# Optimization experiments

Measured on AMD Instinct MI355X. Metric: run time of the kernel, lower is better.

The kernel has to match this reference:

```python
import jax, jax.numpy as jnp
import numpy as np

EMBED_DIM = 512
NUM_TYPES = 26
PER_TYPE = 128
NUM_CODES = NUM_TYPES * PER_TYPE
COMMIT = 0.25
TEMP = 0.07
N_TOKENS = 32768
SAMPLED_PER_TYPE = int(0.1 * PER_TYPE)  # 12


def _normalize(v, axis=-1):
    # matches F.normalize(p=2) with eps clamp
    return v / jnp.clip(jnp.linalg.norm(v, axis=axis, keepdims=True), 1e-12)


def setup_inputs() -> dict:
    key = jax.random.key(0)
    k1, k2, k3, k4 = jax.random.split(key, 4)
    x = jax.random.normal(k1, (N_TOKENS, EMBED_DIM), jnp.float32)
    Q = jax.random.randint(k2, (N_TOKENS,), 0, NUM_TYPES)
    initrange = 1.0 / EMBED_DIM
    emb = jax.random.uniform(k3, (NUM_CODES, EMBED_DIM), jnp.float32, -initrange, initrange)
    emb = _normalize(emb)  # mirrors _initialize_embeddings
    # deterministic stand-in for torch.randperm(num_per_type)[:sampled_num]
    perm = jax.random.permutation(k4, PER_TYPE)[:SAMPLED_PER_TYPE]
    sampled_indices = (jnp.arange(NUM_TYPES)[:, None] * PER_TYPE + perm[None, :]).reshape(-1)
    return {"x": x, "embeddings": emb, "Q": Q, "sampled_indices": sampled_indices}


def _code_indices(xn, embeddings, Q):
    # full [N, num_codes] squared distances, then select the 128-code slab of
    # each token's PTM type and argmin within it (equivalent to the per-type loop)
    d = ((xn ** 2).sum(-1, keepdims=True)
         + (embeddings ** 2).sum(-1)[None, :]
         - 2.0 * (xn @ embeddings.T))                      # [N, NUM_CODES]
    d = d.reshape(xn.shape[0], NUM_TYPES, PER_TYPE)
    d_sel = jnp.take_along_axis(d, Q[:, None, None], axis=1)[:, 0, :]  # [N, PER_TYPE]
    return jnp.argmin(d_sel, axis=1) + Q * PER_TYPE


def _uniform_loss(embeddings, sampled_indices):
    ne = _normalize(embeddings)
    se = ne[sampled_indices]                               # [S, D]
    sim = se @ se.T                                        # [S, S]
    labels = sampled_indices // PER_TYPE
    pos = (labels[None, :] == labels[:, None]).astype(jnp.float32)
    S = sampled_indices.shape[0]
    eye = jnp.eye(S, dtype=bool)
    sim = jnp.where(eye, -jnp.inf, sim)
    sim_exp = jnp.exp(sim / TEMP)                          # exp(-inf) = 0 kills diagonal
    sum_exp = sim_exp.sum(axis=1)
    pos_sum = (sim_exp * pos).sum(axis=1)
    return -jnp.log(pos_sum / sum_exp).mean()


def reference(x, embeddings, Q, sampled_indices):
    xn = _normalize(x)
    idx = _code_indices(xn, embeddings, Q)
    quantized = _normalize(embeddings[idx])
    q_latent = jnp.mean((quantized - jax.lax.stop_gradient(xn)) ** 2)
    e_latent = jnp.mean((xn - jax.lax.stop_gradient(quantized)) ** 2)
    loss = q_latent + COMMIT * e_latent
    uloss = _uniform_loss(embeddings, sampled_indices)
    out = xn + jax.lax.stop_gradient(quantized - xn)       # straight-through
    return out, loss, uloss, idx
```

## Files before the change

### kernel.cpp

```cpp
#include <hip/hip_runtime.h>
#include <math.h>

#define NTOK   32768
#define DIM    512
#define NTYPES 26
#define PT     128
#define NCODES 3328
#define NSAMP  312
#define INV_TEMP (1.0f / 0.07f)
#define MAXTILES 24

typedef __attribute__((ext_vector_type(8))) short short8;
typedef __attribute__((ext_vector_type(4))) float floatx4;

__device__ __forceinline__ void f2bf2(float f, unsigned short& h, unsigned short& l) {
    unsigned u = __float_as_uint(f);
    unsigned hb = (u + 0x7fffu + ((u >> 16) & 1u)) >> 16;
    h = (unsigned short)hb;
    float hf = __uint_as_float(hb << 16);
    float r = f - hf;
    unsigned u2 = __float_as_uint(r);
    l = (unsigned short)((u2 + 0x7fffu + ((u2 >> 16) & 1u)) >> 16);
}

__device__ __forceinline__ void cvt8(float4 a, float4 b, short8& h, short8& l) {
    union { short8 v; unsigned short u[8]; } H, L;
    f2bf2(a.x, H.u[0], L.u[0]); f2bf2(a.y, H.u[1], L.u[1]);
    f2bf2(a.z, H.u[2], L.u[2]); f2bf2(a.w, H.u[3], L.u[3]);
    f2bf2(b.x, H.u[4], L.u[4]); f2bf2(b.y, H.u[5], L.u[5]);
    f2bf2(b.z, H.u[6], L.u[6]); f2bf2(b.w, H.u[7], L.u[7]);
    h = H.v; l = L.v;
}

__device__ __forceinline__ void stage2(const unsigned short* g, unsigned short* l) {
    __builtin_amdgcn_global_load_lds((const __attribute__((address_space(1))) void*)g,
                                     (__attribute__((address_space(3))) void*)l, 16, 0, 0);
    __builtin_amdgcn_global_load_lds((const __attribute__((address_space(1))) void*)(g + 512),
                                     (__attribute__((address_space(3))) void*)(l + 512), 16, 0, 0);
}

__global__ __launch_bounds__(256) void k_pre(const float* __restrict__ emb,
                                             const int* __restrict__ Q,
                                             unsigned short* __restrict__ Bhg,
                                             unsigned short* __restrict__ Blg,
                                             float* __restrict__ sume,
                                             float* __restrict__ rinv,
                                             int* __restrict__ bhist,
                                             int* __restrict__ rankb,
                                             float* __restrict__ accg,
                                             int* __restrict__ donec) {
    int tid = threadIdx.x;
    int bid = blockIdx.x;
    if (bid < NCODES / 4) {
        if (bid == 0) {
            if (tid == 32) accg[0] = 0.0f;
            if (tid == 33) accg[1] = 0.0f;
            if (tid == 34) *donec = 0;
        }
        int wv = tid >> 6, lane = tid & 63;
        int c = bid * 4 + wv;
        const float4* row = (const float4*)(emb + (size_t)c * DIM);
        float4 v0 = row[lane * 2], v1 = row[lane * 2 + 1];
        float s = v0.x*v0.x + v0.y*v0.y + v0.z*v0.z + v0.w*v0.w
                + v1.x*v1.x + v1.y*v1.y + v1.z*v1.z + v1.w*v1.w;
        for (int m = 32; m; m >>= 1) s += __shfl_xor(s, m);
        if (lane == 0) {
            sume[c] = s;
            rinv[c] = 1.0f / fmaxf(sqrtf(s), 1e-12f);
        }
        union { short8 v; unsigned short u[8]; } hh, ll;
        f2bf2(v0.x, hh.u[0], ll.u[0]); f2bf2(v0.y, hh.u[1], ll.u[1]);
        f2bf2(v0.z, hh.u[2], ll.u[2]); f2bf2(v0.w, hh.u[3], ll.u[3]);
        f2bf2(v1.x, hh.u[4], ll.u[4]); f2bf2(v1.y, hh.u[5], ll.u[5]);
        f2bf2(v1.z, hh.u[6], ll.u[6]); f2bf2(v1.w, hh.u[7], ll.u[7]);
        int qq  = c >> 7;
        int n   = c & 127;
        int ni  = n >> 4, lcc = n & 15;
        int ks2 = lane >> 2, q4d = lane & 3;
        size_t dst = (size_t)qq * (PT * DIM)
                   + (size_t)(((ks2 * 8 + ni) * 64 + q4d * 16 + lcc) * 8);
        *(short8*)(Bhg + dst) = hh.v;
        *(short8*)(Blg + dst) = ll.v;
    } else {
        __shared__ int lbin[NTYPES];
        int hb = bid - NCODES / 4;
        if (tid < NTYPES) lbin[tid] = 0;
        __syncthreads();
        int t = hb * 256 + tid;
        int q = Q[t];
        int lr = atomicAdd(&lbin[q], 1);
        __syncthreads();
        if (tid < NTYPES) bhist[hb * 32 + tid] = lbin[tid];
        rankb[t] = lr;
    }
}

__global__ __launch_bounds__(256) void k_scat(const int* __restrict__ Q,
                                              const int* __restrict__ bhist,
                                              const int* __restrict__ rankb,
                                              int* __restrict__ order,
                                              int* __restrict__ offsg) {
    __shared__ int offs_s[NTYPES];
    __shared__ int base_s[NTYPES];
    int b = blockIdx.x;
    int tid = threadIdx.x;
    if (tid < NTYPES) {
        int tot = 0, pre = 0;
        for (int bb = 0; bb < NTOK / 256; bb++) {
            int v = bhist[bb * 32 + tid];
            tot += v;
            if (bb < b) pre += v;
        }
        offs_s[tid] = tot;
        base_s[tid] = pre;
    }
    __syncthreads();
    if (tid == 0) {
        int a = 0;
        for (int t2 = 0; t2 < NTYPES; t2++) {
            int tt = offs_s[t2];
            offs_s[t2] = a;
            if (b == 0) offsg[t2] = a;
            a += tt;
        }
        if (b == 0) offsg[NTYPES] = a;
    }
    __syncthreads();
    int t = b * 256 + tid;
    int q = Q[t];
    order[offs_s[q] + base_s[q] + rankb[t]] = t;
}

#define KSTEP(S, NSTR, AC, AF, DOSTAGE)                                          \
  {                                                                              \
    __builtin_amdgcn_sched_barrier(0);                                           \
    asm volatile("s_waitcnt vmcnt(" NSTR ")" ::: "memory");                      \
    __builtin_amdgcn_s_barrier();                                                \
    __builtin_amdgcn_sched_barrier(0);                                           \
    if (DOSTAGE) {                                                               \
      stage2(bhg + ((S) + 2) * 4096 + stoff, &Bls[((S) + 2) % 3][0][ldoff]);     \
      stage2(blg + ((S) + 2) * 4096 + stoff, &Bls[((S) + 2) % 3][1][ldoff]);     \
      AF[0] = *(const float4*)(ap0 + ((S) + 2) * 32);                            \
      AF[1] = *(const float4*)(ap0 + ((S) + 2) * 32 + 4);                        \
      AF[2] = *(const float4*)(ap1 + ((S) + 2) * 32);                            \
      AF[3] = *(const float4*)(ap1 + ((S) + 2) * 32 + 4);                        \
    }                                                                            \
    __builtin_amdgcn_sched_barrier(0);                                           \
    {                                                                            \
      float4 r0a = AC[0], r0b = AC[1], r1a = AC[2], r1b = AC[3];                 \
      ps0 = fmaf(r0a.x, r0a.x, fmaf(r0a.y, r0a.y, fmaf(r0a.z, r0a.z, fmaf(r0a.w, r0a.w, ps0)))); \
      ps0 = fmaf(r0b.x, r0b.x, fmaf(r0b.y, r0b.y, fmaf(r0b.z, r0b.z, fmaf(r0b.w, r0b.w, ps0)))); \
      ps1 = fmaf(r1a.x, r1a.x, fmaf(r1a.y, r1a.y, fmaf(r1a.z, r1a.z, fmaf(r1a.w, r1a.w, ps1)))); \
      ps1 = fmaf(r1b.x, r1b.x, fmaf(r1b.y, r1b.y, fmaf(r1b.z, r1b.z, fmaf(r1b.w, r1b.w, ps1)))); \
      short8 ah0, al0, ah1, al1;                                                 \
      cvt8(r0a, r0b, ah0, al0);                                                  \
      cvt8(r1a, r1b, ah1, al1);                                                  \
      short8 bhf[4], blf[4];                                                     \
      _Pragma("unroll")                                                          \
      for (int ni = 0; ni < 4; ni++) {                                           \
        bhf[ni] = *(const short8*)&Bls[(S) % 3][0][(wn4 + ni) * 512 + lane8];    \
        blf[ni] = *(const short8*)&Bls[(S) % 3][1][(wn4 + ni) * 512 + lane8];    \
      }                                                                          \
      _Pragma("unroll")                                                          \
      for (int ni = 0; ni < 4; ni++) {                                           \
        acc[0][ni] = __builtin_amdgcn_mfma_f32_16x16x32_bf16(ah0, bhf[ni], acc[0][ni], 0, 0, 0); \
        acc[0][ni] = __builtin_amdgcn_mfma_f32_16x16x32_bf16(ah0, blf[ni], acc[0][ni], 0, 0, 0); \
        acc[0][ni] = __builtin_amdgcn_mfma_f32_16x16x32_bf16(al0, bhf[ni], acc[0][ni], 0, 0, 0); \
        acc[1][ni] = __builtin_amdgcn_mfma_f32_16x16x32_bf16(ah1, bhf[ni], acc[1][ni], 0, 0, 0); \
        acc[1][ni] = __builtin_amdgcn_mfma_f32_16x16x32_bf16(ah1, blf[ni], acc[1][ni], 0, 0, 0); \
        acc[1][ni] = __builtin_amdgcn_mfma_f32_16x16x32_bf16(al1, bhf[ni], acc[1][ni], 0, 0, 0); \
      }                                                                          \
    }                                                                            \
  }

__global__ __launch_bounds__(256, 3) void k_main(const float* __restrict__ x,
                                                 const float* __restrict__ emb,
                                                 const unsigned short* __restrict__ Bhg,
                                                 const unsigned short* __restrict__ Blg,
                                                 const int* __restrict__ order,
                                                 const int* __restrict__ offsg,
                                                 const float* __restrict__ sume,
                                                 const float* __restrict__ rinv,
                                                 float* __restrict__ outbuf,
                                                 float* __restrict__ idxout,
                                                 float* __restrict__ accg) {
    int q = blockIdx.x;
    int tile = blockIdx.y;
    int base = offsg[q];
    int cnt = offsg[q + 1] - base;
    int tstart = tile * 64;
    if (tstart >= cnt) return;
    int nt = min(64, cnt - tstart);

    __shared__ unsigned short Bls[3][2][4096];
    __shared__ int   toks_s[64];
    __shared__ float sume_s[128];
    __shared__ float rinv_s[128];
    __shared__ float redv[64][2];
    __shared__ int   redi[64][2];
    __shared__ int   bestc[64];

    int tid = threadIdx.x;
    int lane = tid & 63;
    int wv = tid >> 6;
    int wm = wv & 1, wn = wv >> 1;
    int lc = lane & 15, q4 = lane >> 4;
    int wn4 = wn * 4, lane8 = lane * 8;
    int stoff = wv * 1024 + lane8;
    int ldoff = wv * 1024;

    if (tid < 64) toks_s[tid] = order[base + tstart + min(tid, nt - 1)];
    if (tid < 128) {
        sume_s[tid] = sume[q * PT + tid];
        rinv_s[tid] = rinv[q * PT + tid];
    }

    int row0 = wm * 32 + lc;
    int tok0 = order[base + tstart + min(row0, nt - 1)];
    int tok1 = order[base + tstart + min(row0 + 16, nt - 1)];
    const float* ap0 = x + (size_t)tok0 * DIM + q4 * 8;
    const float* ap1 = x + (size_t)tok1 * DIM + q4 * 8;

    const unsigned short* bhg = Bhg + (size_t)q * (PT * DIM);
    const unsigned short* blg = Blg + (size_t)q * (PT * DIM);

    floatx4 acc[2][4];
#pragma unroll
    for (int mi = 0; mi < 2; mi++)
#pragma unroll
        for (int ni = 0; ni < 4; ni++)
            acc[mi][ni] = (floatx4){0.f, 0.f, 0.f, 0.f};
    float ps0 = 0.f, ps1 = 0.f;
    float4 Aa[4], Ab[4], Ac[4];

    stage2(bhg + stoff, &Bls[0][0][ldoff]);
    stage2(blg + stoff, &Bls[0][1][ldoff]);
    __builtin_amdgcn_sched_barrier(0);
    Aa[0] = *(const float4*)(ap0);      Aa[1] = *(const float4*)(ap0 + 4);
    Aa[2] = *(const float4*)(ap1);      Aa[3] = *(const float4*)(ap1 + 4);
    __builtin_amdgcn_sched_barrier(0);
    stage2(bhg + 4096 + stoff, &Bls[1][0][ldoff]);
    stage2(blg + 4096 + stoff, &Bls[1][1][ldoff]);
    __builtin_amdgcn_sched_barrier(0);
    Ab[0] = *(const float4*)(ap0 + 32); Ab[1] = *(const float4*)(ap0 + 36);
    Ab[2] = *(const float4*)(ap1 + 32); Ab[3] = *(const float4*)(ap1 + 36);

    KSTEP(0,  "8", Aa, Ac, 1)
    KSTEP(1,  "8", Ab, Aa, 1)
    KSTEP(2,  "8", Ac, Ab, 1)
    KSTEP(3,  "8", Aa, Ac, 1)
    KSTEP(4,  "8", Ab, Aa, 1)
    KSTEP(5,  "8", Ac, Ab, 1)
    KSTEP(6,  "8", Aa, Ac, 1)
    KSTEP(7,  "8", Ab, Aa, 1)
    KSTEP(8,  "8", Ac, Ab, 1)
    KSTEP(9,  "8", Aa, Ac, 1)
    KSTEP(10, "8", Ab, Aa, 1)
    KSTEP(11, "8", Ac, Ab, 1)
    KSTEP(12, "8", Aa, Ac, 1)
    KSTEP(13, "8", Ab, Aa, 1)
    KSTEP(14, "8", Ac, Ab, 0)
    KSTEP(15, "0", Aa, Ab, 0)

    ps0 += __shfl_xor(ps0, 16); ps0 += __shfl_xor(ps0, 32);
    ps1 += __shfl_xor(ps1, 16); ps1 += __shfl_xor(ps1, 32);
    float rn0 = 1.0f / fmaxf(sqrtf(ps0), 1e-12f);
    float rn1 = 1.0f / fmaxf(sqrtf(ps1), 1e-12f);

#pragma unroll
    for (int mi = 0; mi < 2; mi++) {
#pragma unroll
        for (int r = 0; r < 4; r++) {
            int rowrel = q4 * 4 + r;
            float rn = __shfl(mi == 0 ? rn0 : rn1, rowrel);
            float rn2v = -2.0f * rn;
            float bv = 1e30f; int bc = 0;
#pragma unroll
            for (int ni = 0; ni < 4; ni++) {
                int n = wn * 64 + ni * 16 + lc;
                float d = fmaf(rn2v, acc[mi][ni][r], sume_s[n]);
                if (d < bv) { bv = d; bc = n; }
            }
#pragma unroll
            for (int mk = 1; mk <= 8; mk <<= 1) {
                float ov = __shfl_xor(bv, mk);
                int oc = __shfl_xor(bc, mk);
                if (ov < bv || (ov == bv && oc < bc)) { bv = ov; bc = oc; }
            }
            int m = wm * 32 + mi * 16 + rowrel;
            if (lc == 0) { redv[m][wn] = bv; redi[m][wn] = bc; }
        }
    }
    __syncthreads();

    if (tid < 64) {
        float v0 = redv[tid][0], v1 = redv[tid][1];
        int c = (v1 < v0) ? redi[tid][1] : redi[tid][0];
        float bvv = fminf(v0, v1);
        bestc[tid] = c;
        float term = 0.0f;
        if (tid < nt) {
            idxout[toks_s[tid]] = (float)(q * PT + c);
            term = 2.0f - (sume_s[c] - bvv) * rinv_s[c];
        }
        for (int mk = 32; mk; mk >>= 1) term += __shfl_xor(term, mk);
        if (tid == 0) atomicAdd(&accg[0], term);
    }
    __syncthreads();

    for (int t = wv; t < nt; t += 4) {
        int c = bestc[t];
        int gt = toks_s[t];
        float rv = rinv_s[c];
        const float4* er = (const float4*)(emb + (size_t)(q * PT + c) * DIM);
        float4* orow = (float4*)(outbuf + (size_t)gt * DIM);
#pragma unroll
        for (int s2 = 0; s2 < 2; s2++) {
            float4 ev = er[lane * 2 + s2];
            orow[lane * 2 + s2] = make_float4(ev.x * rv, ev.y * rv, ev.z * rv, ev.w * rv);
        }
    }
}

__global__ __launch_bounds__(256) void k_post(const float* __restrict__ emb,
                                              const int* __restrict__ samp,
                                              const float* __restrict__ rinv,
                                              float* __restrict__ accg,
                                              int* __restrict__ donec,
                                              float* __restrict__ lossp) {
    __shared__ float rs[4], rp[4];
    int i = blockIdx.x;
    int tid = threadIdx.x;
    int lane = tid & 63, wv = tid >> 6;
    int ci = samp[i];
    float rvi = rinv[ci];
    int labi = ci >> 7;
    const float4* ri = (const float4*)(emb + (size_t)ci * DIM);
    float4 e0 = ri[lane * 2], e1 = ri[lane * 2 + 1];
    float sE = 0.0f, pE = 0.0f;
    for (int j0 = wv; j0 < NSAMP; j0 += 16) {
        float d[4]; int cj[4]; bool val[4];
#pragma unroll
        for (int u = 0; u < 4; u++) {
            int j = j0 + u * 4;
            val[u] = (j < NSAMP) && (j != i);
            int js = val[u] ? j : 0;
            cj[u] = samp[js];
            const float4* rj = (const float4*)(emb + (size_t)cj[u] * DIM);
            float4 f0 = rj[lane * 2], f1 = rj[lane * 2 + 1];
            d[u] = e0.x*f0.x + e0.y*f0.y + e0.z*f0.z + e0.w*f0.w
                 + e1.x*f1.x + e1.y*f1.y + e1.z*f1.z + e1.w*f1.w;
        }
#pragma unroll
        for (int mk = 32; mk; mk >>= 1)
#pragma unroll
            for (int u = 0; u < 4; u++) d[u] += __shfl_xor(d[u], mk);
#pragma unroll
        for (int u = 0; u < 4; u++) {
            float ex = val[u] ? expf(d[u] * rvi * rinv[cj[u]] * INV_TEMP) : 0.0f;
            sE += ex;
            if (val[u] && (cj[u] >> 7) == labi) pE += ex;
        }
    }
    if (lane == 0) { rs[wv] = sE; rp[wv] = pE; }
    __syncthreads();
    if (tid == 0) {
        float S = rs[0] + rs[1] + rs[2] + rs[3];
        float P = rp[0] + rp[1] + rp[2] + rp[3];
        atomicAdd(&accg[1], logf(S) - logf(P));
        __threadfence();
        int old = atomicAdd(donec, 1);
        if (old == NSAMP - 1) {
            __threadfence();
            float a0 = atomicAdd(&accg[0], 0.0f);
            float a1 = atomicAdd(&accg[1], 0.0f);
            lossp[0] = (1.25f / ((float)NTOK * (float)DIM)) * a0;
            lossp[1] = a1 / (float)NSAMP;
        }
    }
}

extern "C" void kernel_launch(void* const* d_in, const int* in_sizes, int n_in,
                              void* d_out, int out_size, void* d_ws, size_t ws_size,
                              hipStream_t stream) {
    const float* x   = (const float*)d_in[0];
    const float* emb = (const float*)d_in[1];
    const int* Q     = (const int*)d_in[2];
    const int* samp  = (const int*)d_in[3];

    float* out    = (float*)d_out;
    float* lossp  = out + (size_t)NTOK * DIM;
    float* idxout = out + (size_t)NTOK * DIM + 2;

    unsigned short* Bhg = (unsigned short*)d_ws;
    unsigned short* Blg = Bhg + (size_t)NCODES * DIM;
    float* sume  = (float*)(Blg + (size_t)NCODES * DIM);
    float* rinv  = sume + NCODES;
    int* bhist   = (int*)(rinv + NCODES);
    int* rankb   = bhist + (NTOK / 256) * 32;
    int* offsg   = rankb + NTOK;
    int* order   = offsg + NTYPES + 1;
    float* accg  = (float*)(order + NTOK);
    int* donec   = (int*)(accg + 2);

    k_pre<<<NCODES / 4 + NTOK / 256, 256, 0, stream>>>(emb, Q, Bhg, Blg, sume, rinv,
                                                       bhist, rankb, accg, donec);
    k_scat<<<NTOK / 256, 256, 0, stream>>>(Q, bhist, rankb, order, offsg);
    dim3 gmain(NTYPES, MAXTILES);
    k_main<<<gmain, 256, 0, stream>>>(x, emb, Bhg, Blg, order, offsg, sume, rinv,
                                      out, idxout, accg);
    k_post<<<NSAMP, 256, 0, stream>>>(emb, samp, rinv, accg, donec, lossp);
}
```

Measured before the change: 215.6 us.

## Pre-gather tokens into type-sorted bf16 hi/lo buffers and stage A via LDS

Adds a k_gather kernel that reads x once, computes each token's inverse norm, splits it into bf16 hi/lo parts and writes them in type-sorted order into the output buffer, which is used as scratch. k_main then streams A tiles into swizzled LDS with global_load_lds instead of loading fp32 rows into registers and converting inside the K loop. The quantized-row writeback moves from k_main into k_post, which gets extra blocks that read the stored indices. This frees registers in the GEMM loop and removes per-step conversion, at the cost of an extra pass over x, an extra launch, occupancy lowered from 3 to 2 and more LDS.

```diff
diff --git a/kernel.cpp b/kernel.cpp
--- a/kernel.cpp
+++ b/kernel.cpp
@@ -32,11 +32,13 @@
     h = H.v; l = L.v;
 }
 
-__device__ __forceinline__ void stage2(const unsigned short* g, unsigned short* l) {
+__device__ __forceinline__ void gll1(const unsigned short* g, unsigned short* l) {
     __builtin_amdgcn_global_load_lds((const __attribute__((address_space(1))) void*)g,
                                      (__attribute__((address_space(3))) void*)l, 16, 0, 0);
-    __builtin_amdgcn_global_load_lds((const __attribute__((address_space(1))) void*)(g + 512),
-                                     (__attribute__((address_space(3))) void*)(l + 512), 16, 0, 0);
+}
+__device__ __forceinline__ void stage2(const unsigned short* g, unsigned short* l) {
+    gll1(g, l);
+    gll1(g + 512, l + 512);
 }
 
 __global__ __launch_bounds__(256) void k_pre(const float* __restrict__ emb,
@@ -99,6 +101,7 @@
                                               const int* __restrict__ bhist,
                                               const int* __restrict__ rankb,
                                               int* __restrict__ order,
+                                              int* __restrict__ posg,
                                               int* __restrict__ offsg) {
     __shared__ int offs_s[NTYPES];
     __shared__ int base_s[NTYPES];
@@ -128,38 +131,60 @@
     __syncthreads();
     int t = b * 256 + tid;
     int q = Q[t];
-    order[offs_s[q] + base_s[q] + rankb[t]] = t;
-}
-
-#define KSTEP(S, NSTR, AC, AF, DOSTAGE)                                          \
+    int p = offs_s[q] + base_s[q] + rankb[t];
+    order[p] = t;
+    posg[t] = p;
+}
+
+__global__ __launch_bounds__(256) void k_gather(const float* __restrict__ x,
+                                                const int* __restrict__ posg,
+                                                unsigned short* __restrict__ xs_h,
+                                                unsigned short* __restrict__ xs_l,
+                                                float* __restrict__ rn_s_g) {
+    int tid = threadIdx.x, lane = tid & 63, wv = tid >> 6;
+    int tb = blockIdx.x * 64 + wv * 16;
+    int pv = 0;
+    if (lane < 16) pv = posg[tb + lane];
+#pragma unroll 4
+    for (int j = 0; j < 16; j++) {
+        int t = tb + j;
+        const float4* xr = (const float4*)(x + (size_t)t * DIM);
+        float4 f0 = xr[lane * 2], f1 = xr[lane * 2 + 1];
+        float s = f0.x*f0.x + f0.y*f0.y + f0.z*f0.z + f0.w*f0.w
+                + f1.x*f1.x + f1.y*f1.y + f1.z*f1.z + f1.w*f1.w;
+        for (int m = 32; m; m >>= 1) s += __shfl_xor(s, m);
+        int p = __shfl(pv, j);
+        short8 h, l;
+        cvt8(f0, f1, h, l);
+        *(short8*)(xs_h + (size_t)p * DIM + lane * 8) = h;
+        *(short8*)(xs_l + (size_t)p * DIM + lane * 8) = l;
+        if (lane == 0) rn_s_g[p] = 1.0f / fmaxf(sqrtf(s), 1e-12f);
+    }
+}
+
+#define KSTEP(S, NSTR, DOSTAGE)                                                  \
   {                                                                              \
     __builtin_amdgcn_sched_barrier(0);                                           \
     asm volatile("s_waitcnt vmcnt(" NSTR ")" ::: "memory");                      \
     __builtin_amdgcn_s_barrier();                                                \
     __builtin_amdgcn_sched_barrier(0);                                           \
     if (DOSTAGE) {                                                               \
-      stage2(bhg + ((S) + 2) * 4096 + stoff, &Bls[((S) + 2) % 3][0][ldoff]);     \
-      stage2(blg + ((S) + 2) * 4096 + stoff, &Bls[((S) + 2) % 3][1][ldoff]);     \
-      AF[0] = *(const float4*)(ap0 + ((S) + 2) * 32);                            \
-      AF[1] = *(const float4*)(ap0 + ((S) + 2) * 32 + 4);                        \
-      AF[2] = *(const float4*)(ap1 + ((S) + 2) * 32);                            \
-      AF[3] = *(const float4*)(ap1 + ((S) + 2) * 32 + 4);                        \
+      stage2(bhg + ((S) + 2) * 4096 + stoffB, &Bbuf[((S) + 2) % 3][0][ldoffB]);  \
+      stage2(blg + ((S) + 2) * 4096 + stoffB, &Bbuf[((S) + 2) % 3][1][ldoffB]);  \
+      gll1(ash + ((S) + 2) * 32, &Abuf[((S) + 2) % 3][0][ldoffA]);               \
+      gll1(asl + ((S) + 2) * 32, &Abuf[((S) + 2) % 3][1][ldoffA]);               \
     }                                                                            \
     __builtin_amdgcn_sched_barrier(0);                                           \
     {                                                                            \
-      float4 r0a = AC[0], r0b = AC[1], r1a = AC[2], r1b = AC[3];                 \
-      ps0 = fmaf(r0a.x, r0a.x, fmaf(r0a.y, r0a.y, fmaf(r0a.z, r0a.z, fmaf(r0a.w, r0a.w, ps0)))); \
-      ps0 = fmaf(r0b.x, r0b.x, fmaf(r0b.y, r0b.y, fmaf(r0b.z, r0b.z, fmaf(r0b.w, r0b.w, ps0)))); \
-      ps1 = fmaf(r1a.x, r1a.x, fmaf(r1a.y, r1a.y, fmaf(r1a.z, r1a.z, fmaf(r1a.w, r1a.w, ps1)))); \
-      ps1 = fmaf(r1b.x, r1b.x, fmaf(r1b.y, r1b.y, fmaf(r1b.z, r1b.z, fmaf(r1b.w, r1b.w, ps1)))); \
-      short8 ah0, al0, ah1, al1;                                                 \
-      cvt8(r0a, r0b, ah0, al0);                                                  \
-      cvt8(r1a, r1b, ah1, al1);                                                  \
+      short8 ah0 = *(const short8*)&Abuf[(S) % 3][0][aoff0];                     \
+      short8 al0 = *(const short8*)&Abuf[(S) % 3][1][aoff0];                     \
+      short8 ah1 = *(const short8*)&Abuf[(S) % 3][0][aoff1];                     \
+      short8 al1 = *(const short8*)&Abuf[(S) % 3][1][aoff1];                     \
       short8 bhf[4], blf[4];                                                     \
       _Pragma("unroll")                                                          \
       for (int ni = 0; ni < 4; ni++) {                                           \
-        bhf[ni] = *(const short8*)&Bls[(S) % 3][0][(wn4 + ni) * 512 + lane8];    \
-        blf[ni] = *(const short8*)&Bls[(S) % 3][1][(wn4 + ni) * 512 + lane8];    \
+        bhf[ni] = *(const short8*)&Bbuf[(S) % 3][0][(wn4 + ni) * 512 + lane8];   \
+        blf[ni] = *(const short8*)&Bbuf[(S) % 3][1][(wn4 + ni) * 512 + lane8];   \
       }                                                                          \
       _Pragma("unroll")                                                          \
       for (int ni = 0; ni < 4; ni++) {                                           \
@@ -173,15 +198,15 @@
     }                                                                            \
   }
 
-__global__ __launch_bounds__(256, 3) void k_main(const float* __restrict__ x,
-                                                 const float* __restrict__ emb,
+__global__ __launch_bounds__(256, 2) void k_main(const unsigned short* __restrict__ xs_h,
+                                                 const unsigned short* __restrict__ xs_l,
                                                  const unsigned short* __restrict__ Bhg,
                                                  const unsigned short* __restrict__ Blg,
                                                  const int* __restrict__ order,
                                                  const int* __restrict__ offsg,
                                                  const float* __restrict__ sume,
                                                  const float* __restrict__ rinv,
-                                                 float* __restrict__ outbuf,
+                                                 const float* __restrict__ rn_s_g,
                                                  float* __restrict__ idxout,
                                                  float* __restrict__ accg) {
     int q = blockIdx.x;
@@ -192,13 +217,14 @@
     if (tstart >= cnt) return;
     int nt = min(64, cnt - tstart);
 
-    __shared__ unsigned short Bls[3][2][4096];
+    __shared__ __align__(16) unsigned short Bbuf[3][2][4096];
+    __shared__ __align__(16) unsigned short Abuf[3][2][2048];
     __shared__ int   toks_s[64];
     __shared__ float sume_s[128];
     __shared__ float rinv_s[128];
+    __shared__ float rn_sh[64];
     __shared__ float redv[64][2];
     __shared__ int   redi[64][2];
-    __shared__ int   bestc[64];
 
     int tid = threadIdx.x;
     int lane = tid & 63;
@@ -206,79 +232,78 @@
     int wm = wv & 1, wn = wv >> 1;
     int lc = lane & 15, q4 = lane >> 4;
     int wn4 = wn * 4, lane8 = lane * 8;
-    int stoff = wv * 1024 + lane8;
-    int ldoff = wv * 1024;
-
-    if (tid < 64) toks_s[tid] = order[base + tstart + min(tid, nt - 1)];
+    int stoffB = wv * 1024 + lane8;
+    int ldoffB = wv * 1024;
+    int ldoffA = wv * 512;
+
+    if (tid < 64) {
+        toks_s[tid] = order[base + tstart + min(tid, nt - 1)];
+        rn_sh[tid]  = rn_s_g[base + tstart + min(tid, nt - 1)];
+    }
     if (tid < 128) {
         sume_s[tid] = sume[q * PT + tid];
         rinv_s[tid] = rinv[q * PT + tid];
     }
 
-    int row0 = wm * 32 + lc;
-    int tok0 = order[base + tstart + min(row0, nt - 1)];
-    int tok1 = order[base + tstart + min(row0 + 16, nt - 1)];
-    const float* ap0 = x + (size_t)tok0 * DIM + q4 * 8;
-    const float* ap1 = x + (size_t)tok1 * DIM + q4 * 8;
+    int r = tid >> 2, csl = tid & 3;
+    int c_src = csl ^ (r & 3);
+    size_t prow = (size_t)(base + tstart + min(r, nt - 1));
+    const unsigned short* ash = xs_h + prow * DIM + c_src * 8;
+    const unsigned short* asl = xs_l + prow * DIM + c_src * 8;
 
     const unsigned short* bhg = Bhg + (size_t)q * (PT * DIM);
     const unsigned short* blg = Blg + (size_t)q * (PT * DIM);
 
+    int sw = (q4 ^ (lc & 3)) << 3;
+    int aoff0 = (wm * 32 + lc) * 32 + sw;
+    int aoff1 = aoff0 + 16 * 32;
+
     floatx4 acc[2][4];
 #pragma unroll
     for (int mi = 0; mi < 2; mi++)
 #pragma unroll
         for (int ni = 0; ni < 4; ni++)
             acc[mi][ni] = (floatx4){0.f, 0.f, 0.f, 0.f};
-    float ps0 = 0.f, ps1 = 0.f;
-    float4 Aa[4], Ab[4], Ac[4];
-
-    stage2(bhg + stoff, &Bls[0][0][ldoff]);
-    stage2(blg + stoff, &Bls[0][1][ldoff]);
+
+    stage2(bhg + stoffB, &Bbuf[0][0][ldoffB]);
+    stage2(blg + stoffB, &Bbuf[0][1][ldoffB]);
+    gll1(ash, &Abuf[0][0][ldoffA]);
+    gll1(asl, &Abuf[0][1][ldoffA]);
     __builtin_amdgcn_sched_barrier(0);
-    Aa[0] = *(const float4*)(ap0);      Aa[1] = *(const float4*)(ap0 + 4);
-    Aa[2] = *(const float4*)(ap1);      Aa[3] = *(const float4*)(ap1 + 4);
-    __builtin_amdgcn_sched_barrier(0);
-    stage2(bhg + 4096 + stoff, &Bls[1][0][ldoff]);
-    stage2(blg + 4096 + stoff, &Bls[1][1][ldoff]);
-    __builtin_amdgcn_sched_barrier(0);
-    Ab[0] = *(const float4*)(ap0 + 32); Ab[1] = *(const float4*)(ap0 + 36);
-    Ab[2] = *(const float4*)(ap1 + 32); Ab[3] = *(const float4*)(ap1 + 36);
-
-    KSTEP(0,  "8", Aa, Ac, 1)
-    KSTEP(1,  "8", Ab, Aa, 1)
-    KSTEP(2,  "8", Ac, Ab, 1)
-    KSTEP(3,  "8", Aa, Ac, 1)
-    KSTEP(4,  "8", Ab, Aa, 1)
-    KSTEP(5,  "8", Ac, Ab, 1)
-    KSTEP(6,  "8", Aa, Ac, 1)
-    KSTEP(7,  "8", Ab, Aa, 1)
-    KSTEP(8,  "8", Ac, Ab, 1)
-    KSTEP(9,  "8", Aa, Ac, 1)
-    KSTEP(10, "8", Ab, Aa, 1)
-    KSTEP(11, "8", Ac, Ab, 1)
-    KSTEP(12, "8", Aa, Ac, 1)
-    KSTEP(13, "8", Ab, Aa, 1)
-    KSTEP(14, "8", Ac, Ab, 0)
-    KSTEP(15, "0", Aa, Ab, 0)
-
-    ps0 += __shfl_xor(ps0, 16); ps0 += __shfl_xor(ps0, 32);
-    ps1 += __shfl_xor(ps1, 16); ps1 += __shfl_xor(ps1, 32);
-    float rn0 = 1.0f / fmaxf(sqrtf(ps0), 1e-12f);
-    float rn1 = 1.0f / fmaxf(sqrtf(ps1), 1e-12f);
+    stage2(bhg + 4096 + stoffB, &Bbuf[1][0][ldoffB]);
+    stage2(blg + 4096 + stoffB, &Bbuf[1][1][ldoffB]);
+    gll1(ash + 32, &Abuf[1][0][ldoffA]);
+    gll1(asl + 32, &Abuf[1][1][ldoffA]);
+
+    KSTEP(0,  "6", 1)
+    KSTEP(1,  "6", 1)
+    KSTEP(2,  "6", 1)
+    KSTEP(3,  "6", 1)
+    KSTEP(4,  "6", 1)
+    KSTEP(5,  "6", 1)
+    KSTEP(6,  "6", 1)
+    KSTEP(7,  "6", 1)
+    KSTEP(8,  "6", 1)
+    KSTEP(9,  "6", 1)
+    KSTEP(10, "6", 1)
+    KSTEP(11, "6", 1)
+    KSTEP(12, "6", 1)
+    KSTEP(13, "6", 1)
+    KSTEP(14, "6", 0)
+    KSTEP(15, "0", 0)
 
 #pragma unroll
     for (int mi = 0; mi < 2; mi++) {
 #pragma unroll
-        for (int r = 0; r < 4; r++) {
-            int rowrel = q4 * 4 + r;
-            float rn = __shfl(mi == 0 ? rn0 : rn1, rowrel);
-            float rn2v = -2.0f * rn;
+        for (int rr = 0; rr < 4; rr++) {
+            int rowrel = q4 * 4 + rr;
+            int m = wm * 32 + mi * 16 + rowrel;
+            float rn2v = -2.0f * rn_sh[m];
             float bv = 1e30f; int bc = 0;
 #pragma unroll
             for (int ni = 0; ni < 4; ni++) {
                 int n = wn * 64 + ni * 16 + lc;
-                float d = fmaf(rn2v, acc[mi][ni][r], sume_s[n]);
+                float d = fmaf(rn2v, acc[mi][ni][rr], sume_s[n]);
                 if (d < bv) { bv = d; bc = n; }
             }
 #pragma unroll
@@ -287,7 +312,6 @@
                 int oc = __shfl_xor(bc, mk);
                 if (ov < bv || (ov == bv && oc < bc)) { bv = ov; bc = oc; }
             }
-            int m = wm * 32 + mi * 16 + rowrel;
             if (lc == 0) { redv[m][wn] = bv; redi[m][wn] = bc; }
         }
     }
@@ -297,7 +321,6 @@
         float v0 = redv[tid][0], v1 = redv[tid][1];
         int c = (v1 < v0) ? redi[tid][1] : redi[tid][0];
         float bvv = fminf(v0, v1);
-        bestc[tid] = c;
         float term = 0.0f;
         if (tid < nt) {
             idxout[toks_s[tid]] = (float)(q * PT + c);
@@ -306,76 +329,91 @@
         for (int mk = 32; mk; mk >>= 1) term += __shfl_xor(term, mk);
         if (tid == 0) atomicAdd(&accg[0], term);
     }
-    __syncthreads();
-
-    for (int t = wv; t < nt; t += 4) {
-        int c = bestc[t];
-        int gt = toks_s[t];
-        float rv = rinv_s[c];
-        const float4* er = (const float4*)(emb + (size_t)(q * PT + c) * DIM);
-        float4* orow = (float4*)(outbuf + (size_t)gt * DIM);
-#pragma unroll
-        for (int s2 = 0; s2 < 2; s2++) {
-            float4 ev = er[lane * 2 + s2];
-            orow[lane * 2 + s2] = make_float4(ev.x * rv, ev.y * rv, ev.z * rv, ev.w * rv);
-        }
-    }
 }
 
 __global__ __launch_bounds__(256) void k_post(const float* __restrict__ emb,
+                                              const float* __restrict__ rinv,
+                                              const float* __restrict__ idxf,
+                                              float* __restrict__ outbuf,
                                               const int* __restrict__ samp,
-                                              const float* __restrict__ rinv,
                                               float* __restrict__ accg,
                                               int* __restrict__ donec,
                                               float* __restrict__ lossp) {
-    __shared__ float rs[4], rp[4];
-    int i = blockIdx.x;
-    int tid = threadIdx.x;
-    int lane = tid & 63, wv = tid >> 6;
-    int ci = samp[i];
-    float rvi = rinv[ci];
-    int labi = ci >> 7;
-    const float4* ri = (const float4*)(emb + (size_t)ci * DIM);
-    float4 e0 = ri[lane * 2], e1 = ri[lane * 2 + 1];
-    float sE = 0.0f, pE = 0.0f;
-    for (int j0 = wv; j0 < NSAMP; j0 += 16) {
-        float d[4]; int cj[4]; bool val[4];
-#pragma unroll
-        for (int u = 0; u < 4; u++) {
-            int j = j0 + u * 4;
-            val[u] = (j < NSAMP) && (j != i);
-            int js = val[u] ? j : 0;
-            cj[u] = samp[js];
-            const float4* rj = (const float4*)(emb + (size_t)cj[u] * DIM);
-            float4 f0 = rj[lane * 2], f1 = rj[lane * 2 + 1];
-            d[u] = e0.x*f0.x + e0.y*f0.y + e0.z*f0.z + e0.w*f0.w
-                 + e1.x*f1.x + e1.y*f1.y + e1.z*f1.z + e1.w*f1.w;
-        }
-#pragma unroll
-        for (int mk = 32; mk; mk >>= 1)
-#pragma unroll
-            for (int u = 0; u < 4; u++) d[u] += __shfl_xor(d[u], mk);
-#pragma unroll
-        for (int u = 0; u < 4; u++) {
-            float ex = val[u] ? expf(d[u] * rvi * rinv[cj[u]] * INV_TEMP) : 0.0f;
-            sE += ex;
-            if (val[u] && (cj[u] >> 7) == labi) pE += ex;
-        }
-    }
-    if (lane == 0) { rs[wv] = sE; rp[wv] = pE; }
-    __syncthreads();
-    if (tid == 0) {
-        float S = rs[0] + rs[1] + rs[2] + rs[3];
-        float P = rp[0] + rp[1] + rp[2] + rp[3];
-        atomicAdd(&accg[1], logf(S) - logf(P));
-        __threadfence();
-        int old = atomicAdd(donec, 1);
-        if (old == NSAMP - 1) {
+    int bid = blockIdx.x;
+    int tid = threadIdx.x, lane = tid & 63, wv = tid >> 6;
+    if (bid < NTOK / 64) {
+        int tbase = bid * 64 + wv * 16;
+        int cL = 0; float rvL = 0.f;
+        if (lane < 16) {
+            cL = (int)idxf[tbase + lane];
+            rvL = rinv[cL];
+        }
+        const float4* er = (const float4*)emb;
+        int c0 = __shfl(cL, 0); float rv0 = __shfl(rvL, 0);
+        float4 ea = er[(size_t)c0 * 128 + lane * 2];
+        float4 eb = er[(size_t)c0 * 128 + lane * 2 + 1];
+#pragma unroll
+        for (int t = 0; t < 16; t++) {
+            float4 ca = ea, cb = eb;
+            float rv = rv0;
+            if (t < 15) {
+                int c1 = __shfl(cL, t + 1);
+                rv0 = __shfl(rvL, t + 1);
+                ea = er[(size_t)c1 * 128 + lane * 2];
+                eb = er[(size_t)c1 * 128 + lane * 2 + 1];
+            }
+            float4* orow = (float4*)(outbuf + (size_t)(tbase + t) * DIM);
+            orow[lane * 2]     = make_float4(ca.x * rv, ca.y * rv, ca.z * rv, ca.w * rv);
+            orow[lane * 2 + 1] = make_float4(cb.x * rv, cb.y * rv, cb.z * rv, cb.w * rv);
+        }
+    } else {
+        __shared__ float rs[4], rp[4];
+        int i = bid - NTOK / 64;
+        int ci = samp[i];
+        float rvi = rinv[ci];
+        int labi = ci >> 7;
+        const float4* ri = (const float4*)(emb + (size_t)ci * DIM);
+        float4 e0 = ri[lane * 2], e1 = ri[lane * 2 + 1];
+        float sE = 0.0f, pE = 0.0f;
+        for (int j0 = wv; j0 < NSAMP; j0 += 16) {
+            float d[4]; int cj[4]; bool val[4];
+#pragma unroll
+            for (int u = 0; u < 4; u++) {
+                int j = j0 + u * 4;
+                val[u] = (j < NSAMP) && (j != i);
+                int js = val[u] ? j : 0;
+                cj[u] = samp[js];
+                const float4* rj = (const float4*)(emb + (size_t)cj[u] * DIM);
+                float4 f0 = rj[lane * 2], f1 = rj[lane * 2 + 1];
+                d[u] = e0.x*f0.x + e0.y*f0.y + e0.z*f0.z + e0.w*f0.w
+                     + e1.x*f1.x + e1.y*f1.y + e1.z*f1.z + e1.w*f1.w;
+            }
+#pragma unroll
+            for (int mk = 32; mk; mk >>= 1)
+#pragma unroll
+                for (int u = 0; u < 4; u++) d[u] += __shfl_xor(d[u], mk);
+#pragma unroll
+            for (int u = 0; u < 4; u++) {
+                float ex = val[u] ? expf(d[u] * rvi * rinv[cj[u]] * INV_TEMP) : 0.0f;
+                sE += ex;
+                if (val[u] && (cj[u] >> 7) == labi) pE += ex;
+            }
+        }
+        if (lane == 0) { rs[wv] = sE; rp[wv] = pE; }
+        __syncthreads();
+        if (tid == 0) {
+            float S = rs[0] + rs[1] + rs[2] + rs[3];
+            float P = rp[0] + rp[1] + rp[2] + rp[3];
+            atomicAdd(&accg[1], logf(S) - logf(P));
             __threadfence();
-            float a0 = atomicAdd(&accg[0], 0.0f);
-            float a1 = atomicAdd(&accg[1], 0.0f);
-            lossp[0] = (1.25f / ((float)NTOK * (float)DIM)) * a0;
-            lossp[1] = a1 / (float)NSAMP;
+            int old = atomicAdd(donec, 1);
+            if (old == NSAMP - 1) {
+                __threadfence();
+                float a0 = atomicAdd(&accg[0], 0.0f);
+                float a1 = atomicAdd(&accg[1], 0.0f);
+                lossp[0] = (1.25f / ((float)NTOK * (float)DIM)) * a0;
+                lossp[1] = a1 / (float)NSAMP;
+            }
         }
     }
 }
@@ -392,22 +430,29 @@
     float* lossp  = out + (size_t)NTOK * DIM;
     float* idxout = out + (size_t)NTOK * DIM + 2;
 
+    unsigned short* xs_h = (unsigned short*)out;
+    unsigned short* xs_l = xs_h + (size_t)NTOK * DIM;
+
     unsigned short* Bhg = (unsigned short*)d_ws;
     unsigned short* Blg = Bhg + (size_t)NCODES * DIM;
-    float* sume  = (float*)(Blg + (size_t)NCODES * DIM);
-    float* rinv  = sume + NCODES;
-    int* bhist   = (int*)(rinv + NCODES);
-    int* rankb   = bhist + (NTOK / 256) * 32;
-    int* offsg   = rankb + NTOK;
-    int* order   = offsg + NTYPES + 1;
-    float* accg  = (float*)(order + NTOK);
-    int* donec   = (int*)(accg + 2);
+    float* sume   = (float*)(Blg + (size_t)NCODES * DIM);
+    float* rinv   = sume + NCODES;
+    int* bhist    = (int*)(rinv + NCODES);
+    int* rankb    = bhist + (NTOK / 256) * 32;
+    int* posg     = rankb + NTOK;
+    int* offsg    = posg + NTOK;
+    int* order    = offsg + NTYPES + 1;
+    float* rn_s_g = (float*)(order + NTOK);
+    float* accg   = rn_s_g + NTOK;
+    int* donec    = (int*)(accg + 2);
 
     k_pre<<<NCODES / 4 + NTOK / 256, 256, 0, stream>>>(emb, Q, Bhg, Blg, sume, rinv,
                                                        bhist, rankb, accg, donec);
-    k_scat<<<NTOK / 256, 256, 0, stream>>>(Q, bhist, rankb, order, offsg);
+    k_scat<<<NTOK / 256, 256, 0, stream>>>(Q, bhist, rankb, order, posg, offsg);
+    k_gather<<<NTOK / 64, 256, 0, stream>>>(x, posg, xs_h, xs_l, rn_s_g);
     dim3 gmain(NTYPES, MAXTILES);
-    k_main<<<gmain, 256, 0, stream>>>(x, emb, Bhg, Blg, order, offsg, sume, rinv,
-                                      out, idxout, accg);
-    k_post<<<NSAMP, 256, 0, stream>>>(emb, samp, rinv, accg, donec, lossp);
-}
+    k_main<<<gmain, 256, 0, stream>>>(xs_h, xs_l, Bhg, Blg, order, offsg, sume, rinv,
+                                      rn_s_g, idxout, accg);
+    k_post<<<NTOK / 64 + NSAMP, 256, 0, stream>>>(emb, rinv, idxout, out, samp,
+                                                  accg, donec, lossp);
+}
```

Result: slower. 240.1 us (+11.4%).

## Move output row writes to separate coalesced kernel and pre-normalize sampled embeddings

Applied to the files above, without the earlier changes.

The per-token quantized-row write-out leaves the grouped k_main tail and moves into a new k_out kernel. k_out walks tokens in original order, reads the chosen code index back from the idx output, and prefetches the next embedding row while storing the current one. The sampled embeddings are normalized once into a compact workspace buffer inside extra k_scat blocks, so the uniform-loss kernel reads contiguous rows without gathering rinv. This adds one kernel launch and an extra read of the idx buffer, but shortens k_main and makes the 64MB output write sequential.

```diff
diff --git a/kernel.cpp b/kernel.cpp
--- a/kernel.cpp
+++ b/kernel.cpp
@@ -98,37 +98,53 @@
 __global__ __launch_bounds__(256) void k_scat(const int* __restrict__ Q,
                                               const int* __restrict__ bhist,
                                               const int* __restrict__ rankb,
+                                              const float* __restrict__ emb,
+                                              const float* __restrict__ rinv,
+                                              const int* __restrict__ samp,
                                               int* __restrict__ order,
-                                              int* __restrict__ offsg) {
-    __shared__ int offs_s[NTYPES];
-    __shared__ int base_s[NTYPES];
+                                              int* __restrict__ offsg,
+                                              float* __restrict__ ne) {
     int b = blockIdx.x;
     int tid = threadIdx.x;
-    if (tid < NTYPES) {
-        int tot = 0, pre = 0;
-        for (int bb = 0; bb < NTOK / 256; bb++) {
-            int v = bhist[bb * 32 + tid];
-            tot += v;
-            if (bb < b) pre += v;
-        }
-        offs_s[tid] = tot;
-        base_s[tid] = pre;
-    }
-    __syncthreads();
-    if (tid == 0) {
-        int a = 0;
-        for (int t2 = 0; t2 < NTYPES; t2++) {
-            int tt = offs_s[t2];
-            offs_s[t2] = a;
-            if (b == 0) offsg[t2] = a;
-            a += tt;
-        }
-        if (b == 0) offsg[NTYPES] = a;
-    }
-    __syncthreads();
-    int t = b * 256 + tid;
-    int q = Q[t];
-    order[offs_s[q] + base_s[q] + rankb[t]] = t;
+    if (b < NTOK / 256) {
+        __shared__ int offs_s[NTYPES];
+        __shared__ int base_s[NTYPES];
+        if (tid < NTYPES) {
+            int tot = 0, pre = 0;
+            for (int bb = 0; bb < NTOK / 256; bb++) {
+                int v = bhist[bb * 32 + tid];
+                tot += v;
+                if (bb < b) pre += v;
+            }
+            offs_s[tid] = tot;
+            base_s[tid] = pre;
+        }
+        __syncthreads();
+        if (tid == 0) {
+            int a = 0;
+            for (int t2 = 0; t2 < NTYPES; t2++) {
+                int tt = offs_s[t2];
+                offs_s[t2] = a;
+                if (b == 0) offsg[t2] = a;
+                a += tt;
+            }
+            if (b == 0) offsg[NTYPES] = a;
+        }
+        __syncthreads();
+        int t = b * 256 + tid;
+        int q = Q[t];
+        order[offs_s[q] + base_s[q] + rankb[t]] = t;
+    } else {
+        int lane = tid & 63, wv = tid >> 6;
+        int i = (b - NTOK / 256) * 4 + wv;
+        int ci = samp[i];
+        float rv = rinv[ci];
+        const float4* er = (const float4*)(emb + (size_t)ci * DIM);
+        float4 e0 = er[lane * 2], e1 = er[lane * 2 + 1];
+        float4* nr = (float4*)(ne + (size_t)i * DIM);
+        nr[lane * 2]     = make_float4(e0.x * rv, e0.y * rv, e0.z * rv, e0.w * rv);
+        nr[lane * 2 + 1] = make_float4(e1.x * rv, e1.y * rv, e1.z * rv, e1.w * rv);
+    }
 }
 
 #define KSTEP(S, NSTR, AC, AF, DOSTAGE)                                          \
@@ -174,14 +190,12 @@
   }
 
 __global__ __launch_bounds__(256, 3) void k_main(const float* __restrict__ x,
-                                                 const float* __restrict__ emb,
                                                  const unsigned short* __restrict__ Bhg,
                                                  const unsigned short* __restrict__ Blg,
                                                  const int* __restrict__ order,
                                                  const int* __restrict__ offsg,
                                                  const float* __restrict__ sume,
                                                  const float* __restrict__ rinv,
-                                                 float* __restrict__ outbuf,
                                                  float* __restrict__ idxout,
                                                  float* __restrict__ accg) {
     int q = blockIdx.x;
@@ -198,7 +212,6 @@
     __shared__ float rinv_s[128];
     __shared__ float redv[64][2];
     __shared__ int   redi[64][2];
-    __shared__ int   bestc[64];
 
     int tid = threadIdx.x;
     int lane = tid & 63;
@@ -297,7 +310,6 @@
         float v0 = redv[tid][0], v1 = redv[tid][1];
         int c = (v1 < v0) ? redi[tid][1] : redi[tid][0];
         float bvv = fminf(v0, v1);
-        bestc[tid] = c;
         float term = 0.0f;
         if (tid < nt) {
             idxout[toks_s[tid]] = (float)(q * PT + c);
@@ -306,47 +318,61 @@
         for (int mk = 32; mk; mk >>= 1) term += __shfl_xor(term, mk);
         if (tid == 0) atomicAdd(&accg[0], term);
     }
-    __syncthreads();
-
-    for (int t = wv; t < nt; t += 4) {
-        int c = bestc[t];
-        int gt = toks_s[t];
-        float rv = rinv_s[c];
-        const float4* er = (const float4*)(emb + (size_t)(q * PT + c) * DIM);
-        float4* orow = (float4*)(outbuf + (size_t)gt * DIM);
-#pragma unroll
-        for (int s2 = 0; s2 < 2; s2++) {
-            float4 ev = er[lane * 2 + s2];
-            orow[lane * 2 + s2] = make_float4(ev.x * rv, ev.y * rv, ev.z * rv, ev.w * rv);
-        }
-    }
-}
-
-__global__ __launch_bounds__(256) void k_post(const float* __restrict__ emb,
-                                              const int* __restrict__ samp,
-                                              const float* __restrict__ rinv,
-                                              float* __restrict__ accg,
-                                              int* __restrict__ donec,
-                                              float* __restrict__ lossp) {
+}
+
+__global__ __launch_bounds__(256) void k_out(const float* __restrict__ emb,
+                                             const float* __restrict__ rinv,
+                                             const float* __restrict__ idxf,
+                                             float* __restrict__ outbuf) {
+    int tid = threadIdx.x, lane = tid & 63, wv = tid >> 6;
+    int tbase = blockIdx.x * 64 + wv * 16;
+    int cL = 0; float rvL = 0.f;
+    if (lane < 16) {
+        cL = (int)idxf[tbase + lane];
+        rvL = rinv[cL];
+    }
+    const float4* er = (const float4*)emb;
+    int c0 = __shfl(cL, 0); float rv0 = __shfl(rvL, 0);
+    float4 ea = er[(size_t)c0 * 128 + lane * 2];
+    float4 eb = er[(size_t)c0 * 128 + lane * 2 + 1];
+#pragma unroll
+    for (int t = 0; t < 16; t++) {
+        float4 ca = ea, cb = eb;
+        float rv = rv0;
+        if (t < 15) {
+            int c1 = __shfl(cL, t + 1);
+            rv0 = __shfl(rvL, t + 1);
+            ea = er[(size_t)c1 * 128 + lane * 2];
+            eb = er[(size_t)c1 * 128 + lane * 2 + 1];
+        }
+        float4* orow = (float4*)(outbuf + (size_t)(tbase + t) * DIM);
+        orow[lane * 2]     = make_float4(ca.x * rv, ca.y * rv, ca.z * rv, ca.w * rv);
+        orow[lane * 2 + 1] = make_float4(cb.x * rv, cb.y * rv, cb.z * rv, cb.w * rv);
+    }
+}
+
+__global__ __launch_bounds__(256) void k_uloss(const float* __restrict__ ne,
+                                               const int* __restrict__ samp,
+                                               float* __restrict__ accg,
+                                               int* __restrict__ donec,
+                                               float* __restrict__ lossp) {
     __shared__ float rs[4], rp[4];
     int i = blockIdx.x;
     int tid = threadIdx.x;
     int lane = tid & 63, wv = tid >> 6;
-    int ci = samp[i];
-    float rvi = rinv[ci];
-    int labi = ci >> 7;
-    const float4* ri = (const float4*)(emb + (size_t)ci * DIM);
+    int labi = samp[i] >> 7;
+    const float4* ri = (const float4*)(ne + (size_t)i * DIM);
     float4 e0 = ri[lane * 2], e1 = ri[lane * 2 + 1];
     float sE = 0.0f, pE = 0.0f;
     for (int j0 = wv; j0 < NSAMP; j0 += 16) {
-        float d[4]; int cj[4]; bool val[4];
+        float d[4]; int lj[4]; bool val[4];
 #pragma unroll
         for (int u = 0; u < 4; u++) {
             int j = j0 + u * 4;
             val[u] = (j < NSAMP) && (j != i);
             int js = val[u] ? j : 0;
-            cj[u] = samp[js];
-            const float4* rj = (const float4*)(emb + (size_t)cj[u] * DIM);
+            lj[u] = samp[js] >> 7;
+            const float4* rj = (const float4*)(ne + (size_t)js * DIM);
             float4 f0 = rj[lane * 2], f1 = rj[lane * 2 + 1];
             d[u] = e0.x*f0.x + e0.y*f0.y + e0.z*f0.z + e0.w*f0.w
                  + e1.x*f1.x + e1.y*f1.y + e1.z*f1.z + e1.w*f1.w;
@@ -357,9 +383,9 @@
             for (int u = 0; u < 4; u++) d[u] += __shfl_xor(d[u], mk);
 #pragma unroll
         for (int u = 0; u < 4; u++) {
-            float ex = val[u] ? expf(d[u] * rvi * rinv[cj[u]] * INV_TEMP) : 0.0f;
+            float ex = val[u] ? expf(d[u] * INV_TEMP) : 0.0f;
             sE += ex;
-            if (val[u] && (cj[u] >> 7) == labi) pE += ex;
+            if (val[u] && lj[u] == labi) pE += ex;
         }
     }
     if (lane == 0) { rs[wv] = sE; rp[wv] = pE; }
@@ -399,15 +425,18 @@
     int* bhist   = (int*)(rinv + NCODES);
     int* rankb   = bhist + (NTOK / 256) * 32;
     int* offsg   = rankb + NTOK;
-    int* order   = offsg + NTYPES + 1;
-    float* accg  = (float*)(order + NTOK);
+    int* order   = offsg + 32;
+    float* ne    = (float*)(order + NTOK);
+    float* accg  = ne + (size_t)NSAMP * DIM;
     int* donec   = (int*)(accg + 2);
 
     k_pre<<<NCODES / 4 + NTOK / 256, 256, 0, stream>>>(emb, Q, Bhg, Blg, sume, rinv,
                                                        bhist, rankb, accg, donec);
-    k_scat<<<NTOK / 256, 256, 0, stream>>>(Q, bhist, rankb, order, offsg);
+    k_scat<<<NTOK / 256 + NSAMP / 4, 256, 0, stream>>>(Q, bhist, rankb, emb, rinv,
+                                                       samp, order, offsg, ne);
     dim3 gmain(NTYPES, MAXTILES);
-    k_main<<<gmain, 256, 0, stream>>>(x, emb, Bhg, Blg, order, offsg, sume, rinv,
-                                      out, idxout, accg);
-    k_post<<<NSAMP, 256, 0, stream>>>(emb, samp, rinv, accg, donec, lossp);
-}
+    k_main<<<gmain, 256, 0, stream>>>(x, Bhg, Blg, order, offsg, sume, rinv,
+                                      idxout, accg);
+    k_out<<<NTOK / 64, 256, 0, stream>>>(emb, rinv, idxout, out);
+    k_uloss<<<NSAMP, 256, 0, stream>>>(ne, samp, accg, donec, lossp);
+}
```

New measurement: 204.8 us. 5.0% less time.
